# Optimization experiments

Hardware: AMD Instinct MI355X
Metric: run time of the kernel (lower is better)

Reference implementation:

```python
import jax, jax.numpy as jnp
import numpy as np

N = 100000   # nodes
E = 1600000  # directed edges
F_IN = 100
H = 256
N_LABELS = 19
BN_EPS = 1e-5


def setup_inputs() -> dict:
    key = jax.random.key(0)
    ks = jax.random.split(key, 12)
    p = lambda k, shape, s=0.05: jax.random.normal(k, shape, dtype=jnp.float32) * s
    return {
        "x": jax.random.normal(ks[0], (N, F_IN), dtype=jnp.float32),
        "edge_index": jax.random.randint(ks[1], (2, E), 0, N, dtype=jnp.int32),
        "W1": p(ks[2], (F_IN, F_IN)), "b1": jnp.zeros((F_IN,), jnp.float32),
        "W2": p(ks[3], (F_IN, F_IN)), "b2": jnp.zeros((F_IN,), jnp.float32),
        "W3": p(ks[4], (F_IN, H)),   "b3": jnp.zeros((H,), jnp.float32),
        "fc1_W": p(ks[5], (H, H)),   "fc1_b": jnp.zeros((H,), jnp.float32),
        "fc2a_W": p(ks[6], (H, 128)), "fc2a_b": jnp.zeros((128,), jnp.float32),
        "bn_gamma": jnp.ones((128,), jnp.float32), "bn_beta": jnp.zeros((128,), jnp.float32),
        "fc2b_W": p(ks[7], (128, N_LABELS)), "fc2b_b": jnp.zeros((N_LABELS,), jnp.float32),
    }


def _gcn_conv(x, W, b, src, dst, dinv):
    """PyG GCNConv with add_self_loops + symmetric normalization.
    out[dst] += dinv[src]*dinv[dst] * (x @ W)[src], plus self-loop term, plus bias.
    """
    n = x.shape[0]
    xw = x @ W  # [N, out]
    norm = dinv[src] * dinv[dst]  # [E]
    agg = jax.ops.segment_sum(xw[src] * norm[:, None], dst, num_segments=n)
    agg = agg + xw * (dinv * dinv)[:, None]  # self loops (i -> i)
    return agg + b


def reference(x, edge_index, W1, b1, W2, b2, W3, b3, fc1_W, fc1_b,
              fc2a_W, fc2a_b, bn_gamma, bn_beta, fc2b_W, fc2b_b):
    src, dst = edge_index[0], edge_index[1]
    n = x.shape[0]
    # degree of augmented graph (A + I), computed on targets (sum aggregation)
    deg = jax.ops.segment_sum(jnp.ones((src.shape[0],), x.dtype), dst, num_segments=n) + 1.0
    dinv = jax.lax.rsqrt(deg)

    h = jnp.clip(x, -0.4, 0.4)
    h = jax.nn.relu(_gcn_conv(h, W1, b1, src, dst, dinv))
    h = jax.nn.relu(_gcn_conv(h, W2, b2, src, dst, dinv))
    h = jax.nn.relu(_gcn_conv(h, W3, b3, src, dst, dinv))
    h = jax.nn.relu(h @ fc1_W + fc1_b)
    # fc2: Linear -> BatchNorm1d (train mode, batch stats) -> ReLU -> Linear
    h = h @ fc2a_W + fc2a_b
    mu = jnp.mean(h, axis=0)
    var = jnp.mean(jnp.square(h - mu), axis=0)  # biased var, as torch BN uses
    h = (h - mu) * jax.lax.rsqrt(var + BN_EPS) * bn_gamma + bn_beta
    h = jax.nn.relu(h)
    logits = h @ fc2b_W + fc2b_b
    return jax.nn.log_softmax(logits, axis=1)
```

## Files before the change

### kernel.cpp

```cpp
#include <hip/hip_runtime.h>
#include <hip/hip_bf16.h>

#define N_NODES 100000
#define N_EDGES 1600000
#define F_IN_DIM 100
#define F_IN_PAD 104
#define H_DIM 256
#define BN_DIM 128
#define N_LABELS 19
#define BN_EPS 1e-5f
#define M_PAD 100096

#define BUCKET_SHIFT 8
#define NB 391
#define EPB 4096
#define PB 391

typedef __attribute__((ext_vector_type(8))) short bf16x8;
typedef __attribute__((ext_vector_type(4))) short s16x4;
typedef __attribute__((ext_vector_type(4))) float f32x4;

static __device__ inline short f2bf(float f) {
    __hip_bfloat16 h = __float2bfloat16(f);
    return *(short*)&h;
}
static __device__ inline float bf2f(short s) {
    unsigned u = ((unsigned)(unsigned short)s) << 16;
    return __builtin_bit_cast(float, u);
}

#define GLOAD_LDS16(g, l) \
    __builtin_amdgcn_global_load_lds((__attribute__((address_space(1))) const unsigned int*)(g), \
                                     (__attribute__((address_space(3))) unsigned int*)(l), 16, 0, 0)

__global__ __launch_bounds__(256) void part_hist_kernel(const int* __restrict__ dst,
                                                        int* __restrict__ part_hist, int E)
{
    __shared__ int h[NB];
    int tid = threadIdx.x;
    for (int i = tid; i < NB; i += 256) h[i] = 0;
    __syncthreads();
    int base = blockIdx.x * EPB;
    int end = min(base + EPB, E);
    for (int e = base + tid; e < end; e += 256)
        atomicAdd(&h[dst[e] >> BUCKET_SHIFT], 1);
    __syncthreads();
    for (int i = tid; i < NB; i += 256) part_hist[blockIdx.x * NB + i] = h[i];
}

__global__ __launch_bounds__(512) void bucket_total_kernel(const int* __restrict__ part_hist,
                                                           int* __restrict__ bucket_total)
{
    __shared__ int ls[512];
    int b = blockIdx.x;
    int s = 0;
    for (int p = threadIdx.x; p < PB; p += 512) s += part_hist[p * NB + b];
    ls[threadIdx.x] = s;
    __syncthreads();
    for (int off = 256; off > 0; off >>= 1) {
        if (threadIdx.x < off) ls[threadIdx.x] += ls[threadIdx.x + off];
        __syncthreads();
    }
    if (threadIdx.x == 0) bucket_total[b] = ls[0];
}

__global__ __launch_bounds__(512) void bucket_scan_kernel(const int* __restrict__ bucket_total,
                                                          int* __restrict__ bucket_base)
{
    __shared__ int ls[512];
    int tid = threadIdx.x;
    ls[tid] = (tid < NB) ? bucket_total[tid] : 0;
    __syncthreads();
    for (int off = 1; off < 512; off <<= 1) {
        int v = ls[tid];
        int add = (tid >= off) ? ls[tid - off] : 0;
        __syncthreads();
        ls[tid] = v + add;
        __syncthreads();
    }
    if (tid < NB) bucket_base[tid] = (tid > 0) ? ls[tid - 1] : 0;
    if (tid == 0) bucket_base[NB] = ls[NB - 1];
}

__global__ __launch_bounds__(512) void part_offset_kernel(int* __restrict__ part_hist,
                                                          const int* __restrict__ bucket_base)
{
    __shared__ int ls[512];
    int b = blockIdx.x;
    int tid = threadIdx.x;
    int v = (tid < PB) ? part_hist[tid * NB + b] : 0;
    ls[tid] = v;
    __syncthreads();
    for (int off = 1; off < 512; off <<= 1) {
        int x = ls[tid];
        int add = (tid >= off) ? ls[tid - off] : 0;
        __syncthreads();
        ls[tid] = x + add;
        __syncthreads();
    }
    if (tid < PB) part_hist[tid * NB + b] = bucket_base[b] + ((tid > 0) ? ls[tid - 1] : 0);
}

__global__ __launch_bounds__(256) void partition_kernel(const int* __restrict__ src,
                                                        const int* __restrict__ dst,
                                                        const int* __restrict__ part_hist,
                                                        int* __restrict__ ep, int E)
{
    __shared__ int cur[NB];
    int tid = threadIdx.x;
    for (int i = tid; i < NB; i += 256) cur[i] = part_hist[blockIdx.x * NB + i];
    __syncthreads();
    int base = blockIdx.x * EPB;
    int end = min(base + EPB, E);
    for (int e = base + tid; e < end; e += 256) {
        int d = dst[e];
        int s = src[e];
        int pos = atomicAdd(&cur[d >> BUCKET_SHIFT], 1);
        ep[pos] = (s << 8) | (d & 255);
    }
}

__global__ __launch_bounds__(256) void bucket_csr_kernel(const int* __restrict__ ep,
                                                         const int* __restrict__ bucket_base,
                                                         int* __restrict__ row_start,
                                                         float* __restrict__ dinv,
                                                         int* __restrict__ src_sorted, int N, int E)
{
    __shared__ int h[256], sc[256], cur[256];
    int b = blockIdx.x;
    int tid = threadIdx.x;
    int e0 = bucket_base[b], e1 = bucket_base[b + 1];
    int node0 = b << BUCKET_SHIFT;
    int nn = min(256, N - node0);

    h[tid] = 0;
    __syncthreads();
    for (int e = e0 + tid; e < e1; e += 256)
        atomicAdd(&h[ep[e] & 255], 1);
    __syncthreads();

    sc[tid] = h[tid];
    __syncthreads();
    for (int off = 1; off < 256; off <<= 1) {
        int v = sc[tid];
        int add = (tid >= off) ? sc[tid - off] : 0;
        __syncthreads();
        sc[tid] = v + add;
        __syncthreads();
    }
    int excl = e0 + ((tid > 0) ? sc[tid - 1] : 0);
    if (tid < nn) {
        row_start[node0 + tid] = excl;
        dinv[node0 + tid] = rsqrtf((float)h[tid] + 1.0f);
    }
    cur[tid] = excl;
    __syncthreads();
    for (int e = e0 + tid; e < e1; e += 256) {
        int p = ep[e];
        int pos = atomicAdd(&cur[p & 255], 1);
        src_sorted[pos] = ((unsigned)p) >> 8;
    }
    if (b == 0 && tid == 0) row_start[N] = E;
}

__global__ __launch_bounds__(256) void pack_all(
    const float* __restrict__ W1, const float* __restrict__ W2, const float* __restrict__ W3,
    const float* __restrict__ Wf1, const float* __restrict__ Wf2a,
    short* __restrict__ Wt1, short* __restrict__ Wt2, short* __restrict__ Wt3,
    short* __restrict__ Wtf1, short* __restrict__ Wtf2a)
{
    int idx = blockIdx.x * 256 + threadIdx.x;
    const float* W; short* Wt; int K, N, Kp, local;
    if (idx < 10400)       { W = W1;   Wt = Wt1;   K = 100; N = 100; Kp = 104; local = idx; }
    else if (idx < 20800)  { W = W2;   Wt = Wt2;   K = 100; N = 100; Kp = 104; local = idx - 10400; }
    else if (idx < 47424)  { W = W3;   Wt = Wt3;   K = 100; N = 256; Kp = 104; local = idx - 20800; }
    else if (idx < 112960) { W = Wf1;  Wt = Wtf1;  K = 256; N = 256; Kp = 256; local = idx - 47424; }
    else if (idx < 145728) { W = Wf2a; Wt = Wtf2a; K = 256; N = 128; Kp = 256; local = idx - 112960; }
    else return;
    int n = local / Kp, k = local - n * Kp;
    Wt[local] = (k < K) ? f2bf(W[(size_t)k * N + n]) : (short)0;
}

__global__ __launch_bounds__(256) void clip_cast_kernel(const float* __restrict__ x,
                                                        short* __restrict__ xc)
{
    int idx = blockIdx.x * 256 + threadIdx.x;
    if (idx >= N_NODES * 13) return;
    int r = idx / 13, ch = idx - r * 13;
    int c8 = ch * 8;
    const float* xr = x + (size_t)r * F_IN_DIM + c8;
    float v[8];
    float4 v0 = *(const float4*)(xr);
    v[0] = v0.x; v[1] = v0.y; v[2] = v0.z; v[3] = v0.w;
    if (c8 < 96) {
        float4 v1 = *(const float4*)(xr + 4);
        v[4] = v1.x; v[5] = v1.y; v[6] = v1.z; v[7] = v1.w;
    } else {
        v[4] = v[5] = v[6] = v[7] = 0.f;
    }
    bf16x8 o;
    #pragma unroll
    for (int j = 0; j < 8; j++)
        o[j] = f2bf(fminf(fmaxf(v[j], -0.4f), 0.4f));
    *(bf16x8*)(xc + (size_t)r * F_IN_PAD + c8) = o;
}

__global__ __launch_bounds__(256) void gemm_oneshot(
    const short* __restrict__ A,
    const short* __restrict__ Wt,
    const float* __restrict__ bias, const float* __restrict__ rowscale,
    short* __restrict__ C, int M, int Nout, int strideC, int relu)
{
    __shared__ __align__(16) short As[128 * F_IN_PAD];
    __shared__ __align__(16) short Bs[128 * F_IN_PAD];
    int tid = threadIdx.x;
    int wid = tid >> 6;
    int lane = tid & 63;
    int rowBase = blockIdx.x * 128;
    int colBase = blockIdx.y * 128;

    {
        const short* gb = (wid < 2) ? (A + (size_t)rowBase * F_IN_PAD)
                                    : (Wt + (size_t)colBase * F_IN_PAD);
        short* lb = (wid < 2) ? As : Bs;
        int half = (wid & 1) * 13;
        #pragma unroll
        for (int i = 0; i < 13; i++) {
            int c = half + i;
            GLOAD_LDS16(gb + c * 512 + lane * 8, lb + c * 512);
        }
    }
    __syncthreads();

    int quad = lane >> 4, l15 = lane & 15;
    int wave_m = (wid & 1) * 64;
    int wave_n = (wid >> 1) * 64;

    f32x4 acc[4][4];
    #pragma unroll
    for (int i = 0; i < 4; i++)
        #pragma unroll
        for (int j = 0; j < 4; j++)
            acc[i][j] = (f32x4){0.f, 0.f, 0.f, 0.f};

    #pragma unroll
    for (int kc = 0; kc < 4; kc++) {
        int off = kc * 32 + quad * 8;
        bool ok = (off + 8 <= F_IN_PAD);
        bf16x8 a[4], b[4];
        #pragma unroll
        for (int im = 0; im < 4; im++)
            a[im] = ok ? *(const bf16x8*)(As + (wave_m + im * 16 + l15) * F_IN_PAD + off)
                       : (bf16x8){0,0,0,0,0,0,0,0};
        #pragma unroll
        for (int in = 0; in < 4; in++)
            b[in] = ok ? *(const bf16x8*)(Bs + (wave_n + in * 16 + l15) * F_IN_PAD + off)
                       : (bf16x8){0,0,0,0,0,0,0,0};
        #pragma unroll
        for (int im = 0; im < 4; im++)
            #pragma unroll
            for (int in = 0; in < 4; in++)
                acc[im][in] = __builtin_amdgcn_mfma_f32_16x16x32_bf16(
                    a[im], b[in], acc[im][in], 0, 0, 0);
    }

    #pragma unroll
    for (int im = 0; im < 4; im++) {
        #pragma unroll
        for (int reg = 0; reg < 4; reg++) {
            int row = rowBase + wave_m + im * 16 + quad * 4 + reg;
            if (row >= M) continue;
            float rs = rowscale ? rowscale[row] : 1.f;
            #pragma unroll
            for (int in = 0; in < 4; in++) {
                int col = colBase + wave_n + in * 16 + l15;
                if (col >= strideC) continue;
                float v = 0.f;
                if (col < Nout) {
                    v = acc[im][in][reg];
                    if (bias) v += bias[col];
                    v *= rs;
                    if (relu) v = fmaxf(v, 0.f);
                }
                C[(size_t)row * strideC + col] = f2bf(v);
            }
        }
    }
}

__global__ __launch_bounds__(512, 4) void fc_fused_kernel(
    const short* __restrict__ A,
    const short* __restrict__ W1t,
    const float* __restrict__ b1v,
    const short* __restrict__ W2t,
    const float* __restrict__ b2v,
    short* __restrict__ C)
{
    __shared__ __align__(16) short SB[128 * 256];
    int tid = threadIdx.x;
    int wid = tid >> 6;
    int lane = tid & 63;
    int quad = lane >> 4, l15 = lane & 15;
    int rowBase = blockIdx.x * 128;
    int xr = (l15 & 7) << 4;

    #pragma unroll
    for (int i = 0; i < 8; i++) {
        int c = i * 8 + wid;
        int r = c * 2 + (lane >> 5);
        int pb = ((lane & 31) * 16) ^ ((r & 7) << 4);
        const short* gp = A + (size_t)(rowBase + r) * H_DIM + (pb >> 1);
        GLOAD_LDS16(gp, SB + c * 512);
    }

    int wm = (wid & 1) * 64;
    int wn = (wid >> 1) * 64;

    f32x4 acc[4][4];
    #pragma unroll
    for (int i = 0; i < 4; i++)
        #pragma unroll
        for (int j = 0; j < 4; j++)
            acc[i][j] = (f32x4){0.f, 0.f, 0.f, 0.f};

    bf16x8 bA[4], bB[4];
    auto g1loadB = [&](bf16x8 (&dst)[4], int ks) {
        #pragma unroll
        for (int in = 0; in < 4; in++)
            dst[in] = *(const bf16x8*)(W1t + (size_t)(wn + in * 16 + l15) * H_DIM
                                       + ks * 32 + quad * 8);
    };
    auto g1step = [&](bf16x8 (&bc)[4], int ks) {
        bf16x8 a_[4];
        #pragma unroll
        for (int im = 0; im < 4; im++)
            a_[im] = *(const bf16x8*)(SB + (wm + im * 16 + l15) * 256
                                      + (((ks * 64 + quad * 16) ^ xr) >> 1));
        #pragma unroll
        for (int im = 0; im < 4; im++)
            #pragma unroll
            for (int in = 0; in < 4; in++)
                acc[im][in] = __builtin_amdgcn_mfma_f32_16x16x32_bf16(
                    bc[in], a_[im], acc[im][in], 0, 0, 0);
    };

    g1loadB(bA, 0);
    __syncthreads();

    g1loadB(bB, 1); g1step(bA, 0);
    g1loadB(bA, 2); g1step(bB, 1);
    g1loadB(bB, 3); g1step(bA, 2);
    g1loadB(bA, 4); g1step(bB, 3);
    g1loadB(bB, 5); g1step(bA, 4);
    g1loadB(bA, 6); g1step(bB, 5);
    g1loadB(bB, 7); g1step(bA, 6);
    g1step(bB, 7);

    float bb1[4][4];
    #pragma unroll
    for (int in = 0; in < 4; in++)
        #pragma unroll
        for (int r = 0; r < 4; r++)
            bb1[in][r] = b1v[wn + in * 16 + quad * 4 + r];

    __syncthreads();

    int wm2 = (wid & 1) * 64;
    int wn2 = (wid >> 1) * 32;
    bf16x8 cA[2], cB[2];
    auto g2loadB = [&](bf16x8 (&dst)[2], int ks) {
        #pragma unroll
        for (int in = 0; in < 2; in++)
            dst[in] = *(const bf16x8*)(W2t + (size_t)(wn2 + in * 16 + l15) * H_DIM
                                       + ks * 32 + quad * 8);
    };
    g2loadB(cA, 0);
    float bb2[2] = { b2v[wn2 + l15], b2v[wn2 + 16 + l15] };

    #pragma unroll
    for (int im = 0; im < 4; im++) {
        int ml = wm + im * 16 + l15;
        #pragma unroll
        for (int in = 0; in < 4; in++) {
            int nb = (wn + in * 16 + quad * 4) * 2;
            s16x4 o = (s16x4){
                f2bf(fmaxf(acc[im][in][0] + bb1[in][0], 0.f)),
                f2bf(fmaxf(acc[im][in][1] + bb1[in][1], 0.f)),
                f2bf(fmaxf(acc[im][in][2] + bb1[in][2], 0.f)),
                f2bf(fmaxf(acc[im][in][3] + bb1[in][3], 0.f))};
            *(s16x4*)(SB + ml * 256 + ((nb ^ xr) >> 1)) = o;
        }
    }
    __syncthreads();

    f32x4 acc2[4][2];
    #pragma unroll
    for (int i = 0; i < 4; i++)
        #pragma unroll
        for (int j = 0; j < 2; j++)
            acc2[i][j] = (f32x4){0.f, 0.f, 0.f, 0.f};

    auto g2step = [&](bf16x8 (&bc)[2], int ks) {
        bf16x8 a_[4];
        #pragma unroll
        for (int im = 0; im < 4; im++)
            a_[im] = *(const bf16x8*)(SB + (wm2 + im * 16 + l15) * 256
                                      + (((ks * 64 + quad * 16) ^ xr) >> 1));
        #pragma unroll
        for (int im = 0; im < 4; im++)
            #pragma unroll
            for (int in = 0; in < 2; in++)
                acc2[im][in] = __builtin_amdgcn_mfma_f32_16x16x32_bf16(
                    a_[im], bc[in], acc2[im][in], 0, 0, 0);
    };

    g2loadB(cB, 1); g2step(cA, 0);
    g2loadB(cA, 2); g2step(cB, 1);
    g2loadB(cB, 3); g2step(cA, 2);
    g2loadB(cA, 4); g2step(cB, 3);
    g2loadB(cB, 5); g2step(cA, 4);
    g2loadB(cA, 6); g2step(cB, 5);
    g2loadB(cB, 7); g2step(cA, 6);
    g2step(cB, 7);

    #pragma unroll
    for (int im = 0; im < 4; im++) {
        #pragma unroll
        for (int reg = 0; reg < 4; reg++) {
            int row = rowBase + wm2 + im * 16 + quad * 4 + reg;
            #pragma unroll
            for (int in = 0; in < 2; in++) {
                int col = wn2 + in * 16 + l15;
                C[(size_t)row * BN_DIM + col] = f2bf(acc2[im][in][reg] + bb2[in]);
            }
        }
    }
}

template<int F, int STRIDE, int T, int MODE>
__global__ void gather_kernel(const short* __restrict__ xws,
                              const int* __restrict__ row_start,
                              const int* __restrict__ src_sorted,
                              const float* __restrict__ dinv,
                              const float* __restrict__ bias,
                              short* __restrict__ out, int n)
{
    constexpr int CHUNKS = STRIDE / 8;
    int group = (blockIdx.x * blockDim.x + threadIdx.x) / T;
    int lane = threadIdx.x % T;
    if (group >= n || lane >= CHUNKS) return;
    int d = group;
    int e0 = row_start[d], e1 = row_start[d + 1];
    int coff = lane * 8;
    const short* base = xws + coff;

    float acc[8] = {}, acc2[8] = {};
    int e = e0;
    for (; e + 3 < e1; e += 4) {
        int s0 = src_sorted[e + 0];
        int s1 = src_sorted[e + 1];
        int s2 = src_sorted[e + 2];
        int s3 = src_sorted[e + 3];
        bf16x8 v0 = *(const bf16x8*)(base + (size_t)s0 * STRIDE);
        bf16x8 v1 = *(const bf16x8*)(base + (size_t)s1 * STRIDE);
        bf16x8 v2 = *(const bf16x8*)(base + (size_t)s2 * STRIDE);
        bf16x8 v3 = *(const bf16x8*)(base + (size_t)s3 * STRIDE);
        #pragma unroll
        for (int j = 0; j < 8; j++) {
            acc[j]  += bf2f(v0[j]) + bf2f(v2[j]);
            acc2[j] += bf2f(v1[j]) + bf2f(v3[j]);
        }
    }
    for (; e < e1; e++) {
        int s = src_sorted[e];
        bf16x8 v = *(const bf16x8*)(base + (size_t)s * STRIDE);
        #pragma unroll
        for (int j = 0; j < 8; j++) acc[j] += bf2f(v[j]);
    }

    bf16x8 xv = *(const bf16x8*)(xws + (size_t)d * STRIDE + coff);
    float di = dinv[d];
    bf16x8 o;
    #pragma unroll
    for (int j = 0; j < 8; j++) {
        int col = coff + j;
        float v = 0.f;
        if (col < F) {
            v = di * (acc[j] + acc2[j] + bf2f(xv[j]));
            if (MODE == 0) v = fmaxf(v + bias[col], 0.f);
            if (MODE == 1) v = di * fmaxf(v + bias[col], 0.f);
        }
        o[j] = f2bf(v);
    }
    *(bf16x8*)(out + (size_t)d * STRIDE + coff) = o;
}

__global__ void bn_stats_kernel(const short* __restrict__ h,
                                float* __restrict__ sum, float* __restrict__ sumsq, int Ntot)
{
    int c = threadIdx.x & 127;
    int rpb = blockDim.x >> 7;
    int r0 = blockIdx.x * rpb + (threadIdx.x >> 7);
    int stride = gridDim.x * rpb;
    float s = 0.f, ss = 0.f;
    for (int r = r0; r < Ntot; r += stride) {
        float v = bf2f(h[(size_t)r * BN_DIM + c]);
        s += v; ss += v * v;
    }
    __shared__ float ls[256], lss[256];
    ls[threadIdx.x] = s; lss[threadIdx.x] = ss;
    __syncthreads();
    if (threadIdx.x < 128) {
        s = ls[threadIdx.x] + ls[threadIdx.x + 128];
        ss = lss[threadIdx.x] + lss[threadIdx.x + 128];
        atomicAdd(&sum[c], s);
        atomicAdd(&sumsq[c], ss);
    }
}

__global__ void bn_finalize_kernel(const float* __restrict__ sum, const float* __restrict__ sumsq,
                                   const float* __restrict__ gamma, const float* __restrict__ beta,
                                   float* __restrict__ a, float* __restrict__ b, int Ntot)
{
    int c = threadIdx.x;
    float inv_n = 1.0f / (float)Ntot;
    float mu = sum[c] * inv_n;
    float var = sumsq[c] * inv_n - mu * mu;
    float ai = gamma[c] * rsqrtf(var + BN_EPS);
    a[c] = ai;
    b[c] = beta[c] - mu * ai;
}

__global__ __launch_bounds__(256) void fc2b_fused_kernel(
    const short* __restrict__ h, const float* __restrict__ bn_a, const float* __restrict__ bn_b,
    const float* __restrict__ W, const float* __restrict__ bias,
    float* __restrict__ out, int Ntot)
{
    __shared__ float Ws[BN_DIM][N_LABELS + 1];
    __shared__ float as[BN_DIM], bs[BN_DIM];
    for (int i = threadIdx.x; i < BN_DIM * N_LABELS; i += 256) {
        int k = i / N_LABELS, j = i - k * N_LABELS;
        Ws[k][j] = W[i];
    }
    if (threadIdx.x < BN_DIM) {
        as[threadIdx.x] = bn_a[threadIdx.x];
        bs[threadIdx.x] = bn_b[threadIdx.x];
    }
    __syncthreads();

    int r = blockIdx.x * 256 + threadIdx.x;
    if (r >= Ntot) return;

    float acc[N_LABELS];
    #pragma unroll
    for (int j = 0; j < N_LABELS; j++) acc[j] = bias[j];

    const short* hr = h + (size_t)r * BN_DIM;
    #pragma unroll
    for (int k0 = 0; k0 < BN_DIM; k0 += 8) {
        bf16x8 hv = *(const bf16x8*)(hr + k0);
        #pragma unroll
        for (int t = 0; t < 8; t++) {
            float v = fmaxf(bf2f(hv[t]) * as[k0 + t] + bs[k0 + t], 0.f);
            #pragma unroll
            for (int j = 0; j < N_LABELS; j++)
                acc[j] = fmaf(v, Ws[k0 + t][j], acc[j]);
        }
    }

    float m = acc[0];
    #pragma unroll
    for (int j = 1; j < N_LABELS; j++) m = fmaxf(m, acc[j]);
    float s = 0.f;
    #pragma unroll
    for (int j = 0; j < N_LABELS; j++) s += expf(acc[j] - m);
    float lse = m + logf(s);
    float* o = out + (size_t)r * N_LABELS;
    #pragma unroll
    for (int j = 0; j < N_LABELS; j++) o[j] = acc[j] - lse;
}

extern "C" void kernel_launch(void* const* d_in, const int* in_sizes, int n_in,
                              void* d_out, int out_size, void* d_ws, size_t ws_size,
                              hipStream_t stream)
{
    const float* x      = (const float*)d_in[0];
    const int*   ei     = (const int*)d_in[1];
    const float* W1     = (const float*)d_in[2];
    const float* b1     = (const float*)d_in[3];
    const float* W2     = (const float*)d_in[4];
    const float* b2     = (const float*)d_in[5];
    const float* W3     = (const float*)d_in[6];
    const float* b3     = (const float*)d_in[7];
    const float* fc1_W  = (const float*)d_in[8];
    const float* fc1_b  = (const float*)d_in[9];
    const float* fc2aW  = (const float*)d_in[10];
    const float* fc2ab  = (const float*)d_in[11];
    const float* gamma  = (const float*)d_in[12];
    const float* beta   = (const float*)d_in[13];
    const float* fc2bW  = (const float*)d_in[14];
    const float* fc2bb  = (const float*)d_in[15];
    float* out = (float*)d_out;

    const int* src = ei;
    const int* dst = ei + N_EDGES;

    char* w = (char*)d_ws;
    float* dinv        = (float*)w;  w += ((size_t)N_NODES * 4 + 255) / 256 * 256;
    int*   row_start   = (int*)w;    w += ((size_t)(N_NODES + 1) * 4 + 255) / 256 * 256;
    int*   part_hist   = (int*)w;    w += ((size_t)PB * NB * 4 + 255) / 256 * 256;
    int*   bucket_total= (int*)w;    w += ((size_t)NB * 4 + 255) / 256 * 256;
    int*   bucket_base = (int*)w;    w += ((size_t)(NB + 1) * 4 + 255) / 256 * 256;
    float* bn_sum      = (float*)w;  w += 128 * 4;
    float* bn_sumsq    = (float*)w;  w += 128 * 4;
    float* bn_a        = (float*)w;  w += 128 * 4;
    float* bn_b        = (float*)w;  w += 128 * 4;
    short* Wt1         = (short*)w;  w += ((size_t)F_IN_DIM * F_IN_PAD * 2 + 255) / 256 * 256;
    short* Wt2         = (short*)w;  w += ((size_t)F_IN_DIM * F_IN_PAD * 2 + 255) / 256 * 256;
    short* Wt3         = (short*)w;  w += ((size_t)H_DIM * F_IN_PAD * 2 + 255) / 256 * 256;
    short* Wtf1        = (short*)w;  w += ((size_t)H_DIM * H_DIM * 2 + 255) / 256 * 256;
    short* Wtf2a       = (short*)w;  w += ((size_t)BN_DIM * H_DIM * 2 + 255) / 256 * 256;
    int*   src_sorted  = (int*)w;    w += ((size_t)N_EDGES * 4 + 255) / 256 * 256;
    int*   ep          = (int*)w;    w += ((size_t)N_EDGES * 4 + 255) / 256 * 256;
    short* xws100      = (short*)w;  w += ((size_t)M_PAD * F_IN_PAD * 2 + 255) / 256 * 256;
    short* agg100      = (short*)w;  w += ((size_t)M_PAD * F_IN_PAD * 2 + 255) / 256 * 256;
    short* big1        = (short*)w;  w += ((size_t)M_PAD * H_DIM * 2 + 255) / 256 * 256;
    short* big2        = (short*)w;  w += ((size_t)M_PAD * H_DIM * 2 + 255) / 256 * 256;

    short* xclip = big1;

    part_hist_kernel<<<PB, 256, 0, stream>>>(dst, part_hist, N_EDGES);
    bucket_total_kernel<<<NB, 512, 0, stream>>>(part_hist, bucket_total);
    bucket_scan_kernel<<<1, 512, 0, stream>>>(bucket_total, bucket_base);
    part_offset_kernel<<<NB, 512, 0, stream>>>(part_hist, bucket_base);
    partition_kernel<<<PB, 256, 0, stream>>>(src, dst, part_hist, ep, N_EDGES);
    bucket_csr_kernel<<<NB, 256, 0, stream>>>(ep, bucket_base, row_start, dinv,
                                              src_sorted, N_NODES, N_EDGES);

    pack_all<<<570, 256, 0, stream>>>(W1, W2, W3, fc1_W, fc2aW, Wt1, Wt2, Wt3, Wtf1, Wtf2a);
    clip_cast_kernel<<<(N_NODES * 13 + 255) / 256, 256, 0, stream>>>(x, xclip);

    const int nOne = (N_NODES + 127) / 128;
    int gatherBlocks = (N_NODES * 16 + 255) / 256;

    gemm_oneshot<<<dim3(nOne, 1), 256, 0, stream>>>(
        xclip, Wt1, nullptr, dinv, xws100, N_NODES, F_IN_DIM, F_IN_PAD, 0);
    gather_kernel<F_IN_DIM, F_IN_PAD, 16, 0><<<gatherBlocks, 256, 0, stream>>>(
        xws100, row_start, src_sorted, dinv, b1, agg100, N_NODES);

    gemm_oneshot<<<dim3(nOne, 1), 256, 0, stream>>>(
        agg100, Wt2, nullptr, dinv, xws100, N_NODES, F_IN_DIM, F_IN_PAD, 0);
    gather_kernel<F_IN_DIM, F_IN_PAD, 16, 1><<<gatherBlocks, 256, 0, stream>>>(
        xws100, row_start, src_sorted, dinv, b2, agg100, N_NODES);

    gather_kernel<F_IN_DIM, F_IN_PAD, 16, 2><<<gatherBlocks, 256, 0, stream>>>(
        agg100, row_start, src_sorted, dinv, nullptr, xws100, N_NODES);
    gemm_oneshot<<<dim3(nOne, 2), 256, 0, stream>>>(
        xws100, Wt3, b3, nullptr, big1, N_NODES, H_DIM, H_DIM, 1);

    fc_fused_kernel<<<nOne, 512, 0, stream>>>(
        big1, Wtf1, fc1_b, Wtf2a, fc2ab, big2);

    hipMemsetAsync(bn_sum, 0, 2 * 128 * 4, stream);
    bn_stats_kernel<<<512, 256, 0, stream>>>(big2, bn_sum, bn_sumsq, N_NODES);
    bn_finalize_kernel<<<1, 128, 0, stream>>>(bn_sum, bn_sumsq, gamma, beta, bn_a, bn_b, N_NODES);

    fc2b_fused_kernel<<<(N_NODES + 255) / 256, 256, 0, stream>>>(
        big2, bn_a, bn_b, fc2bW, fc2bb, out, N_NODES);
}
```

Measured before the change: 591.7 us.

## Merge CSR build into cooperative kernel and fold small prep/BN kernels

Replaces six CSR-construction kernels with a single cooperative-launch kernel that uses grid-wide syncs between phases. It also merges weight packing with the input clip/cast, zeroes the BN accumulators inside fc_fused instead of issuing a memset, and computes the BN finalize inside fc2b. The goal is fewer kernel launches and less inter-kernel gap overhead. In exchange, the cooperative launch needs all 391 blocks of 512 threads to be resident at once, and BN finalize is now redone in every fc2b block.

```diff
diff --git a/kernel.cpp b/kernel.cpp
--- a/kernel.cpp
+++ b/kernel.cpp
@@ -1,5 +1,8 @@
 #include <hip/hip_runtime.h>
 #include <hip/hip_bf16.h>
+#include <hip/hip_cooperative_groups.h>
+
+namespace cg = cooperative_groups;
 
 #define N_NODES 100000
 #define N_EDGES 1600000
@@ -16,6 +19,9 @@
 #define EPB 4096
 #define PB 391
 
+#define PACK_TOTAL 145728
+#define CLIP_TOTAL (N_NODES * 13)
+
 typedef __attribute__((ext_vector_type(8))) short bf16x8;
 typedef __attribute__((ext_vector_type(4))) short s16x4;
 typedef __attribute__((ext_vector_type(4))) float f32x4;
@@ -33,160 +39,144 @@
     __builtin_amdgcn_global_load_lds((__attribute__((address_space(1))) const unsigned int*)(g), \
                                      (__attribute__((address_space(3))) unsigned int*)(l), 16, 0, 0)
 
-__global__ __launch_bounds__(256) void part_hist_kernel(const int* __restrict__ dst,
-                                                        int* __restrict__ part_hist, int E)
-{
-    __shared__ int h[NB];
-    int tid = threadIdx.x;
-    for (int i = tid; i < NB; i += 256) h[i] = 0;
-    __syncthreads();
-    int base = blockIdx.x * EPB;
-    int end = min(base + EPB, E);
-    for (int e = base + tid; e < end; e += 256)
-        atomicAdd(&h[dst[e] >> BUCKET_SHIFT], 1);
-    __syncthreads();
-    for (int i = tid; i < NB; i += 256) part_hist[blockIdx.x * NB + i] = h[i];
-}
-
-__global__ __launch_bounds__(512) void bucket_total_kernel(const int* __restrict__ part_hist,
-                                                           int* __restrict__ bucket_total)
-{
-    __shared__ int ls[512];
-    int b = blockIdx.x;
-    int s = 0;
-    for (int p = threadIdx.x; p < PB; p += 512) s += part_hist[p * NB + b];
-    ls[threadIdx.x] = s;
-    __syncthreads();
-    for (int off = 256; off > 0; off >>= 1) {
-        if (threadIdx.x < off) ls[threadIdx.x] += ls[threadIdx.x + off];
-        __syncthreads();
-    }
-    if (threadIdx.x == 0) bucket_total[b] = ls[0];
-}
-
-__global__ __launch_bounds__(512) void bucket_scan_kernel(const int* __restrict__ bucket_total,
-                                                          int* __restrict__ bucket_base)
-{
-    __shared__ int ls[512];
-    int tid = threadIdx.x;
-    ls[tid] = (tid < NB) ? bucket_total[tid] : 0;
-    __syncthreads();
-    for (int off = 1; off < 512; off <<= 1) {
-        int v = ls[tid];
-        int add = (tid >= off) ? ls[tid - off] : 0;
-        __syncthreads();
-        ls[tid] = v + add;
-        __syncthreads();
-    }
-    if (tid < NB) bucket_base[tid] = (tid > 0) ? ls[tid - 1] : 0;
-    if (tid == 0) bucket_base[NB] = ls[NB - 1];
-}
-
-__global__ __launch_bounds__(512) void part_offset_kernel(int* __restrict__ part_hist,
-                                                          const int* __restrict__ bucket_base)
-{
-    __shared__ int ls[512];
+__global__ __launch_bounds__(512) void csr_coop_kernel(
+    const int* __restrict__ src, const int* __restrict__ dst,
+    int* __restrict__ part_hist, int* __restrict__ bucket_total,
+    int* __restrict__ bucket_base, int* __restrict__ row_start,
+    float* __restrict__ dinv, int* __restrict__ ep, int* __restrict__ src_sorted)
+{
+    cg::grid_group grid = cg::this_grid();
     int b = blockIdx.x;
     int tid = threadIdx.x;
-    int v = (tid < PB) ? part_hist[tid * NB + b] : 0;
-    ls[tid] = v;
-    __syncthreads();
-    for (int off = 1; off < 512; off <<= 1) {
-        int x = ls[tid];
-        int add = (tid >= off) ? ls[tid - off] : 0;
-        __syncthreads();
-        ls[tid] = x + add;
-        __syncthreads();
-    }
-    if (tid < PB) part_hist[tid * NB + b] = bucket_base[b] + ((tid > 0) ? ls[tid - 1] : 0);
-}
-
-__global__ __launch_bounds__(256) void partition_kernel(const int* __restrict__ src,
-                                                        const int* __restrict__ dst,
-                                                        const int* __restrict__ part_hist,
-                                                        int* __restrict__ ep, int E)
-{
-    __shared__ int cur[NB];
-    int tid = threadIdx.x;
-    for (int i = tid; i < NB; i += 256) cur[i] = part_hist[blockIdx.x * NB + i];
-    __syncthreads();
-    int base = blockIdx.x * EPB;
-    int end = min(base + EPB, E);
-    for (int e = base + tid; e < end; e += 256) {
-        int d = dst[e];
-        int s = src[e];
-        int pos = atomicAdd(&cur[d >> BUCKET_SHIFT], 1);
-        ep[pos] = (s << 8) | (d & 255);
-    }
-}
-
-__global__ __launch_bounds__(256) void bucket_csr_kernel(const int* __restrict__ ep,
-                                                         const int* __restrict__ bucket_base,
-                                                         int* __restrict__ row_start,
-                                                         float* __restrict__ dinv,
-                                                         int* __restrict__ src_sorted, int N, int E)
-{
-    __shared__ int h[256], sc[256], cur[256];
-    int b = blockIdx.x;
-    int tid = threadIdx.x;
-    int e0 = bucket_base[b], e1 = bucket_base[b + 1];
-    int node0 = b << BUCKET_SHIFT;
-    int nn = min(256, N - node0);
-
-    h[tid] = 0;
-    __syncthreads();
-    for (int e = e0 + tid; e < e1; e += 256)
-        atomicAdd(&h[ep[e] & 255], 1);
-    __syncthreads();
-
-    sc[tid] = h[tid];
-    __syncthreads();
-    for (int off = 1; off < 256; off <<= 1) {
-        int v = sc[tid];
-        int add = (tid >= off) ? sc[tid - off] : 0;
-        __syncthreads();
-        sc[tid] = v + add;
-        __syncthreads();
-    }
-    int excl = e0 + ((tid > 0) ? sc[tid - 1] : 0);
-    if (tid < nn) {
-        row_start[node0 + tid] = excl;
-        dinv[node0 + tid] = rsqrtf((float)h[tid] + 1.0f);
-    }
-    cur[tid] = excl;
-    __syncthreads();
-    for (int e = e0 + tid; e < e1; e += 256) {
-        int p = ep[e];
-        int pos = atomicAdd(&cur[p & 255], 1);
-        src_sorted[pos] = ((unsigned)p) >> 8;
-    }
-    if (b == 0 && tid == 0) row_start[N] = E;
-}
-
-__global__ __launch_bounds__(256) void pack_all(
+
+    __shared__ int sh[512];
+    __shared__ int h2[256], cur[256];
+
+    for (int i = tid; i < NB; i += 512) sh[i] = 0;
+    __syncthreads();
+    {
+        int base = b * EPB;
+        int end = min(base + EPB, N_EDGES);
+        for (int e = base + tid; e < end; e += 512)
+            atomicAdd(&sh[dst[e] >> BUCKET_SHIFT], 1);
+    }
+    __syncthreads();
+    for (int i = tid; i < NB; i += 512) part_hist[b * NB + i] = sh[i];
+    grid.sync();
+
+    {
+        int s = 0;
+        for (int p = tid; p < PB; p += 512) s += part_hist[p * NB + b];
+        __syncthreads();
+        sh[tid] = s;
+        __syncthreads();
+        for (int off = 256; off > 0; off >>= 1) {
+            if (tid < off) sh[tid] += sh[tid + off];
+            __syncthreads();
+        }
+        if (tid == 0) bucket_total[b] = sh[0];
+    }
+    grid.sync();
+
+    if (b == 0) {
+        sh[tid] = (tid < NB) ? bucket_total[tid] : 0;
+        __syncthreads();
+        for (int off = 1; off < 512; off <<= 1) {
+            int v = sh[tid];
+            int add = (tid >= off) ? sh[tid - off] : 0;
+            __syncthreads();
+            sh[tid] = v + add;
+            __syncthreads();
+        }
+        if (tid < NB) bucket_base[tid] = (tid > 0) ? sh[tid - 1] : 0;
+        if (tid == 0) bucket_base[NB] = sh[NB - 1];
+    }
+    grid.sync();
+
+    {
+        int v = (tid < PB) ? part_hist[tid * NB + b] : 0;
+        sh[tid] = v;
+        __syncthreads();
+        for (int off = 1; off < 512; off <<= 1) {
+            int x = sh[tid];
+            int add = (tid >= off) ? sh[tid - off] : 0;
+            __syncthreads();
+            sh[tid] = x + add;
+            __syncthreads();
+        }
+        if (tid < PB) part_hist[tid * NB + b] = bucket_base[b] + ((tid > 0) ? sh[tid - 1] : 0);
+    }
+    grid.sync();
+
+    for (int i = tid; i < NB; i += 512) sh[i] = part_hist[b * NB + i];
+    __syncthreads();
+    {
+        int base = b * EPB;
+        int end = min(base + EPB, N_EDGES);
+        for (int e = base + tid; e < end; e += 512) {
+            int d = dst[e];
+            int s = src[e];
+            int pos = atomicAdd(&sh[d >> BUCKET_SHIFT], 1);
+            ep[pos] = (s << 8) | (d & 255);
+        }
+    }
+    grid.sync();
+
+    {
+        int e0 = bucket_base[b], e1 = bucket_base[b + 1];
+        int node0 = b << BUCKET_SHIFT;
+        int nn = min(256, N_NODES - node0);
+        if (tid < 256) h2[tid] = 0;
+        __syncthreads();
+        for (int e = e0 + tid; e < e1; e += 512)
+            atomicAdd(&h2[ep[e] & 255], 1);
+        __syncthreads();
+        sh[tid] = (tid < 256) ? h2[tid] : 0;
+        __syncthreads();
+        for (int off = 1; off < 256; off <<= 1) {
+            int v = sh[tid];
+            int add = (tid >= off && tid < 256) ? sh[tid - off] : 0;
+            __syncthreads();
+            if (tid < 256) sh[tid] = v + add;
+            __syncthreads();
+        }
+        int excl = e0 + ((tid > 0 && tid <= 256) ? sh[tid - 1] : 0);
+        if (tid < nn) {
+            row_start[node0 + tid] = excl;
+            dinv[node0 + tid] = rsqrtf((float)h2[tid] + 1.0f);
+        }
+        if (tid < 256) cur[tid] = excl;
+        __syncthreads();
+        for (int e = e0 + tid; e < e1; e += 512) {
+            int p = ep[e];
+            int pos = atomicAdd(&cur[p & 255], 1);
+            src_sorted[pos] = ((unsigned)p) >> 8;
+        }
+        if (b == 0 && tid == 0) row_start[N_NODES] = N_EDGES;
+    }
+}
+
+__global__ __launch_bounds__(256) void prep_kernel(
     const float* __restrict__ W1, const float* __restrict__ W2, const float* __restrict__ W3,
-    const float* __restrict__ Wf1, const float* __restrict__ Wf2a,
+    const float* __restrict__ Wf1, const float* __restrict__ Wf2a, const float* __restrict__ x,
     short* __restrict__ Wt1, short* __restrict__ Wt2, short* __restrict__ Wt3,
-    short* __restrict__ Wtf1, short* __restrict__ Wtf2a)
+    short* __restrict__ Wtf1, short* __restrict__ Wtf2a, short* __restrict__ xc)
 {
     int idx = blockIdx.x * 256 + threadIdx.x;
-    const float* W; short* Wt; int K, N, Kp, local;
-    if (idx < 10400)       { W = W1;   Wt = Wt1;   K = 100; N = 100; Kp = 104; local = idx; }
-    else if (idx < 20800)  { W = W2;   Wt = Wt2;   K = 100; N = 100; Kp = 104; local = idx - 10400; }
-    else if (idx < 47424)  { W = W3;   Wt = Wt3;   K = 100; N = 256; Kp = 104; local = idx - 20800; }
-    else if (idx < 112960) { W = Wf1;  Wt = Wtf1;  K = 256; N = 256; Kp = 256; local = idx - 47424; }
-    else if (idx < 145728) { W = Wf2a; Wt = Wtf2a; K = 256; N = 128; Kp = 256; local = idx - 112960; }
-    else return;
-    int n = local / Kp, k = local - n * Kp;
-    Wt[local] = (k < K) ? f2bf(W[(size_t)k * N + n]) : (short)0;
-}
-
-__global__ __launch_bounds__(256) void clip_cast_kernel(const float* __restrict__ x,
-                                                        short* __restrict__ xc)
-{
-    int idx = blockIdx.x * 256 + threadIdx.x;
-    if (idx >= N_NODES * 13) return;
-    int r = idx / 13, ch = idx - r * 13;
+    if (idx < PACK_TOTAL) {
+        const float* W; short* Wt; int K, N, Kp, local;
+        if (idx < 10400)       { W = W1;   Wt = Wt1;   K = 100; N = 100; Kp = 104; local = idx; }
+        else if (idx < 20800)  { W = W2;   Wt = Wt2;   K = 100; N = 100; Kp = 104; local = idx - 10400; }
+        else if (idx < 47424)  { W = W3;   Wt = Wt3;   K = 100; N = 256; Kp = 104; local = idx - 20800; }
+        else if (idx < 112960) { W = Wf1;  Wt = Wtf1;  K = 256; N = 256; Kp = 256; local = idx - 47424; }
+        else                   { W = Wf2a; Wt = Wtf2a; K = 256; N = 128; Kp = 256; local = idx - 112960; }
+        int n = local / Kp, k = local - n * Kp;
+        Wt[local] = (k < K) ? f2bf(W[(size_t)k * N + n]) : (short)0;
+        return;
+    }
+    int cidx = idx - PACK_TOTAL;
+    if (cidx >= CLIP_TOTAL) return;
+    int r = cidx / 13, ch = cidx - r * 13;
     int c8 = ch * 8;
     const float* xr = x + (size_t)r * F_IN_DIM + c8;
     float v[8];
@@ -294,7 +284,8 @@
     const float* __restrict__ b1v,
     const short* __restrict__ W2t,
     const float* __restrict__ b2v,
-    short* __restrict__ C)
+    short* __restrict__ C,
+    float* __restrict__ bn_stats)
 {
     __shared__ __align__(16) short SB[128 * 256];
     int tid = threadIdx.x;
@@ -303,6 +294,8 @@
     int quad = lane >> 4, l15 = lane & 15;
     int rowBase = blockIdx.x * 128;
     int xr = (l15 & 7) << 4;
+
+    if (blockIdx.x == 0 && tid < 256) bn_stats[tid] = 0.f;
 
     #pragma unroll
     for (int i = 0; i < 8; i++) {
@@ -518,21 +511,9 @@
     }
 }
 
-__global__ void bn_finalize_kernel(const float* __restrict__ sum, const float* __restrict__ sumsq,
-                                   const float* __restrict__ gamma, const float* __restrict__ beta,
-                                   float* __restrict__ a, float* __restrict__ b, int Ntot)
-{
-    int c = threadIdx.x;
-    float inv_n = 1.0f / (float)Ntot;
-    float mu = sum[c] * inv_n;
-    float var = sumsq[c] * inv_n - mu * mu;
-    float ai = gamma[c] * rsqrtf(var + BN_EPS);
-    a[c] = ai;
-    b[c] = beta[c] - mu * ai;
-}
-
 __global__ __launch_bounds__(256) void fc2b_fused_kernel(
-    const short* __restrict__ h, const float* __restrict__ bn_a, const float* __restrict__ bn_b,
+    const short* __restrict__ h, const float* __restrict__ bn_sum, const float* __restrict__ bn_sumsq,
+    const float* __restrict__ gamma, const float* __restrict__ beta,
     const float* __restrict__ W, const float* __restrict__ bias,
     float* __restrict__ out, int Ntot)
 {
@@ -543,8 +524,13 @@
         Ws[k][j] = W[i];
     }
     if (threadIdx.x < BN_DIM) {
-        as[threadIdx.x] = bn_a[threadIdx.x];
-        bs[threadIdx.x] = bn_b[threadIdx.x];
+        int c = threadIdx.x;
+        float inv_n = 1.0f / (float)Ntot;
+        float mu = bn_sum[c] * inv_n;
+        float var = bn_sumsq[c] * inv_n - mu * mu;
+        float ai = gamma[c] * rsqrtf(var + BN_EPS);
+        as[c] = ai;
+        bs[c] = beta[c] - mu * ai;
     }
     __syncthreads();
 
@@ -613,8 +599,6 @@
     int*   bucket_base = (int*)w;    w += ((size_t)(NB + 1) * 4 + 255) / 256 * 256;
     float* bn_sum      = (float*)w;  w += 128 * 4;
     float* bn_sumsq    = (float*)w;  w += 128 * 4;
-    float* bn_a        = (float*)w;  w += 128 * 4;
-    float* bn_b        = (float*)w;  w += 128 * 4;
     short* Wt1         = (short*)w;  w += ((size_t)F_IN_DIM * F_IN_PAD * 2 + 255) / 256 * 256;
     short* Wt2         = (short*)w;  w += ((size_t)F_IN_DIM * F_IN_PAD * 2 + 255) / 256 * 256;
     short* Wt3         = (short*)w;  w += ((size_t)H_DIM * F_IN_PAD * 2 + 255) / 256 * 256;
@@ -629,16 +613,16 @@
 
     short* xclip = big1;
 
-    part_hist_kernel<<<PB, 256, 0, stream>>>(dst, part_hist, N_EDGES);
-    bucket_total_kernel<<<NB, 512, 0, stream>>>(part_hist, bucket_total);
-    bucket_scan_kernel<<<1, 512, 0, stream>>>(bucket_total, bucket_base);
-    part_offset_kernel<<<NB, 512, 0, stream>>>(part_hist, bucket_base);
-    partition_kernel<<<PB, 256, 0, stream>>>(src, dst, part_hist, ep, N_EDGES);
-    bucket_csr_kernel<<<NB, 256, 0, stream>>>(ep, bucket_base, row_start, dinv,
-                                              src_sorted, N_NODES, N_EDGES);
-
-    pack_all<<<570, 256, 0, stream>>>(W1, W2, W3, fc1_W, fc2aW, Wt1, Wt2, Wt3, Wtf1, Wtf2a);
-    clip_cast_kernel<<<(N_NODES * 13 + 255) / 256, 256, 0, stream>>>(x, xclip);
+    {
+        void* cargs[] = {(void*)&src, (void*)&dst, (void*)&part_hist, (void*)&bucket_total,
+                         (void*)&bucket_base, (void*)&row_start, (void*)&dinv,
+                         (void*)&ep, (void*)&src_sorted};
+        hipLaunchCooperativeKernel((void*)csr_coop_kernel, dim3(NB), dim3(512),
+                                   cargs, 0, stream);
+    }
+
+    prep_kernel<<<(PACK_TOTAL + CLIP_TOTAL + 255) / 256, 256, 0, stream>>>(
+        W1, W2, W3, fc1_W, fc2aW, x, Wt1, Wt2, Wt3, Wtf1, Wtf2a, xclip);
 
     const int nOne = (N_NODES + 127) / 128;
     int gatherBlocks = (N_NODES * 16 + 255) / 256;
@@ -659,12 +643,10 @@
         xws100, Wt3, b3, nullptr, big1, N_NODES, H_DIM, H_DIM, 1);
 
     fc_fused_kernel<<<nOne, 512, 0, stream>>>(
-        big1, Wtf1, fc1_b, Wtf2a, fc2ab, big2);
-
-    hipMemsetAsync(bn_sum, 0, 2 * 128 * 4, stream);
+        big1, Wtf1, fc1_b, Wtf2a, fc2ab, big2, bn_sum);
+
     bn_stats_kernel<<<512, 256, 0, stream>>>(big2, bn_sum, bn_sumsq, N_NODES);
-    bn_finalize_kernel<<<1, 128, 0, stream>>>(bn_sum, bn_sumsq, gamma, beta, bn_a, bn_b, N_NODES);
 
     fc2b_fused_kernel<<<(N_NODES + 255) / 256, 256, 0, stream>>>(
-        big2, bn_a, bn_b, fc2bW, fc2bb, out, N_NODES);
-}
+        big2, bn_sum, bn_sumsq, gamma, beta, fc2bW, fc2bb, out, N_NODES);
+}
```

Measured after the change: 853.4 us. 1.44x slower.
